# Performance work log

Hardware: AMD Instinct MI355X
Metric: run time of the kernel (lower is better)

Reference implementation:

```python
import jax, jax.numpy as jnp
import numpy as np

N_NODES = 50000
N_EDGES = 800000


def gcn_layer(x, edge_index, W, b):
    """PyG-style GCNConv: add self-loops, symmetric deg^-1/2 normalization,
    linear transform, scatter-sum aggregation at target nodes, plus bias."""
    n = x.shape[0]
    loops = jnp.arange(n)
    src = jnp.concatenate([edge_index[0], loops])  # [E+N]
    dst = jnp.concatenate([edge_index[1], loops])  # [E+N]
    deg = jax.ops.segment_sum(jnp.ones(src.shape, dtype=x.dtype), dst, num_segments=n)
    dinv = jnp.where(deg > 0, jax.lax.rsqrt(deg), jnp.zeros((), x.dtype))
    norm = dinv[src] * dinv[dst]               # [E+N]
    h = x @ W                                   # [N, out]
    msg = norm[:, None] * h[src]                # [E+N, out] gather
    out = jax.ops.segment_sum(msg, dst, num_segments=n)  # scatter-add
    return out + b


def setup_inputs() -> dict:
    key = jax.random.key(0)
    ks = jax.random.split(key, 8)
    features = jax.random.normal(ks[0], (N_NODES, 64), dtype=jnp.float32)
    edge_index1 = jax.random.randint(ks[1], (2, N_EDGES), 0, N_NODES)
    edge_index3 = jax.random.randint(ks[2], (2, N_EDGES), 0, N_NODES)
    edge_index9 = jax.random.randint(ks[3], (2, N_EDGES), 0, N_NODES)

    def glorot(k, fi, fo):
        lim = float(np.sqrt(6.0 / (fi + fo)))
        return jax.random.uniform(k, (fi, fo), minval=-lim, maxval=lim, dtype=jnp.float32)

    W1 = glorot(ks[4], 64, 64)
    W2 = glorot(ks[5], 64, 32)
    W3 = glorot(ks[6], 32, 16)
    b1 = jnp.zeros((64,), jnp.float32)
    b2 = jnp.zeros((32,), jnp.float32)
    b3 = jnp.zeros((16,), jnp.float32)
    return dict(features=features, edge_index1=edge_index1, edge_index3=edge_index3,
                edge_index9=edge_index9, W1=W1, b1=b1, W2=W2, b2=b2, W3=W3, b3=b3)


def reference(features, edge_index1, edge_index3, edge_index9, W1, b1, W2, b2, W3, b3):
    x = jax.nn.relu(gcn_layer(features, edge_index1, W1, b1))  # hop 1
    x = jax.nn.relu(gcn_layer(x, edge_index3, W2, b2))         # hop 3
    x = jax.nn.relu(gcn_layer(x, edge_index9, W3, b3))         # hop 9
    return x
```

## Files before the change

kernel.cpp:

```cpp
#include <hip/hip_runtime.h>
#include <hip/hip_fp16.h>


#define NB   256
#define NL   3
#define TB   (NB * NL)
#define CAPE 6400
#define CAPE_E (CAPE + 8)
#define CH   8192
#define P1T  512
#define EPT  (CH / P1T)
#define P2T  512

__device__ __forceinline__ void decode_chunk(int g, int nc1, int nc2,
                                             const int* s1, const int* d1, int E1,
                                             const int* s2, const int* d2, int E2,
                                             const int* s3, const int* d3, int E3,
                                             const int** src, const int** dst, int* E, int* l,
                                             int* gout) {
    if (g < nc1)            { *src = s1; *dst = d1; *E = E1; *l = 0; }
    else if (g < nc1 + nc2) { *src = s2; *dst = d2; *E = E2; *l = 1; g -= nc1; }
    else                    { *src = s3; *dst = d3; *E = E3; *l = 2; g -= nc1 + nc2; }
    *gout = g;
}

__device__ __forceinline__ void fma4(float4& a, float s, const float4& w) {
    a.x += s * w.x; a.y += s * w.y; a.z += s * w.z; a.w += s * w.w;
}
__device__ __forceinline__ void add4(float4& a, const float4& v) {
    a.x += v.x; a.y += v.y; a.z += v.z; a.w += v.w;
}
__device__ __forceinline__ float4 ldh4(const __half* h, size_t idx4) {
    uint2 r = ((const uint2*)h)[idx4];
    __half2 a = *reinterpret_cast<__half2*>(&r.x);
    __half2 b = *reinterpret_cast<__half2*>(&r.y);
    float2 fa = __half22float2(a), fb = __half22float2(b);
    return make_float4(fa.x, fa.y, fb.x, fb.y);
}
__device__ __forceinline__ void sth4(__half* h, size_t idx4, float4 v) {
    __half2 a = __floats2half2_rn(v.x, v.y);
    __half2 b = __floats2half2_rn(v.z, v.w);
    uint2 r;
    r.x = *reinterpret_cast<unsigned*>(&a);
    r.y = *reinterpret_cast<unsigned*>(&b);
    ((uint2*)h)[idx4] = r;
}

__global__ void __launch_bounds__(P1T) k1_phase1_gemm1(
        const int* __restrict__ s1, const int* __restrict__ d1, int E1,
        const int* __restrict__ s2, const int* __restrict__ d2, int E2,
        const int* __restrict__ s3, const int* __restrict__ d3, int E3,
        int nc1, int nc2, int W, int nchunks,
        int* __restrict__ gcur, unsigned int* __restrict__ pairBuf,
        const float* __restrict__ x0, const float* __restrict__ W1g,
        __half* __restrict__ h1) {
    __shared__ __align__(16) char smem[45056];
    const int t = threadIdx.x;
    if (blockIdx.x < (unsigned)nchunks) {
        int* hist = (int*)smem;
        int* eofs = hist + NB;
        int* bo   = eofs + NB;
        int* lcur = bo + NB;
        unsigned* stage = (unsigned*)(smem + 4096);
        unsigned char* stageQ = (unsigned char*)(smem + 36864);
        for (int i = t; i < NB; i += P1T) hist[i] = 0;
        __syncthreads();
        const int* src; const int* dst; int E, l, g;
        decode_chunk(blockIdx.x, nc1, nc2, s1, d1, E1, s2, d2, E2, s3, d3, E3,
                     &src, &dst, &E, &l, &g);
        const int e0 = g * CH;
        const int lbase = l * NB;
        unsigned pv[EPT];
        int bn[EPT];
        if (E - e0 >= CH) {
            const int4* s4 = (const int4*)(src + e0);
            const int4* d4 = (const int4*)(dst + e0);
#pragma unroll
            for (int w = 0; w < EPT / 4; ++w) {
                int4 sv = s4[t + w * P1T];
                int4 dv = d4[t + w * P1T];
                int q, i = w * 4;
                q = dv.x / W; bn[i+0] = q; pv[i+0] = ((unsigned)sv.x << 9) | (unsigned)(dv.x - q * W);
                q = dv.y / W; bn[i+1] = q; pv[i+1] = ((unsigned)sv.y << 9) | (unsigned)(dv.y - q * W);
                q = dv.z / W; bn[i+2] = q; pv[i+2] = ((unsigned)sv.z << 9) | (unsigned)(dv.z - q * W);
                q = dv.w / W; bn[i+3] = q; pv[i+3] = ((unsigned)sv.w << 9) | (unsigned)(dv.w - q * W);
            }
        } else {
#pragma unroll
            for (int i = 0; i < EPT; ++i) {
                int e = e0 + t + i * P1T;
                if (e < E) {
                    int s = src[e], d = dst[e];
                    int q = d / W;
                    bn[i] = q;
                    pv[i] = ((unsigned)s << 9) | (unsigned)(d - q * W);
                } else bn[i] = -1;
            }
        }
#pragma unroll
        for (int i = 0; i < EPT; ++i)
            if (bn[i] >= 0) atomicAdd(&hist[bn[i]], 1);
        __syncthreads();
        if (t < NB) eofs[t] = hist[t];
        __syncthreads();
        for (int off = 1; off < NB; off <<= 1) {
            int add = (t < NB && t >= off) ? eofs[t - off] : 0;
            __syncthreads();
            if (t < NB) eofs[t] += add;
            __syncthreads();
        }
        const int total = eofs[NB - 1];
        int excl = 0;
        if (t < NB) excl = eofs[t] - hist[t];
        __syncthreads();
        if (t < NB) {
            eofs[t] = excl;
            lcur[t] = excl;
            int c = hist[t];
            bo[t] = (lbase + t) * CAPE + (c ? atomicAdd(&gcur[lbase + t], c) : 0);
        }
        __syncthreads();
#pragma unroll
        for (int i = 0; i < EPT; ++i) {
            if (bn[i] >= 0) {
                int r = atomicAdd(&lcur[bn[i]], 1);
                stage[r] = pv[i];
                stageQ[r] = (unsigned char)bn[i];
            }
        }
        __syncthreads();
        for (int i = t; i < total; i += P1T) {
            int q = stageQ[i];
            int k = bo[q] + (i - eofs[q]);
            if (k < (lbase + q + 1) * CAPE) pairBuf[k] = stage[i];
        }
    } else {
        float* Ws = (float*)smem;
        const int bid = blockIdx.x - nchunks;
        for (int i = t; i < 1024; i += P1T)
            ((float4*)Ws)[i] = ((const float4*)W1g)[i];
        __syncthreads();
        const int tc = t % 16;
        const int tr = t / 16;
        const int row0 = bid * 128 + tr * 4;
        const float4* x4 = (const float4*)x0;
        const float4* Ws4 = (const float4*)Ws;
        float4 acc[4];
#pragma unroll
        for (int r = 0; r < 4; ++r) acc[r] = make_float4(0.f, 0.f, 0.f, 0.f);
        int rowc[4];
#pragma unroll
        for (int r = 0; r < 4; ++r) rowc[r] = min(row0 + r, 49999);
        for (int k0 = 0; k0 < 64; k0 += 4) {
            float4 wv0 = Ws4[(k0 + 0) * 16 + tc];
            float4 wv1 = Ws4[(k0 + 1) * 16 + tc];
            float4 wv2 = Ws4[(k0 + 2) * 16 + tc];
            float4 wv3 = Ws4[(k0 + 3) * 16 + tc];
#pragma unroll
            for (int r = 0; r < 4; ++r) {
                float4 xv = x4[(size_t)rowc[r] * 16 + (k0 / 4)];
                fma4(acc[r], xv.x, wv0);
                fma4(acc[r], xv.y, wv1);
                fma4(acc[r], xv.z, wv2);
                fma4(acc[r], xv.w, wv3);
            }
        }
#pragma unroll
        for (int r = 0; r < 4; ++r) {
            int row = row0 + r;
            if (row < 50000) sth4(h1, (size_t)row * 16 + tc, acc[r]);
        }
    }
}

__global__ void __launch_bounds__(P2T) k2_phase2(
        const unsigned int* __restrict__ pairBuf, const int* __restrict__ gcur,
        int n, int W,
        int* __restrict__ row_ptr, int* __restrict__ cnt_g,
        float* __restrict__ dinv, unsigned short* __restrict__ eidx,
        __half* __restrict__ h1, int* __restrict__ perm) {
    __shared__ __align__(16) char smem[20480];
    int* lcnt  = (int*)smem;
    int* lscan = lcnt + P2T;
    unsigned short* stage = (unsigned short*)(lscan + P2T);
    float* dloc = (float*)(smem + 17408);
    unsigned* sortk = (unsigned*)(smem + 19456);
    const int bid = blockIdx.x;
    const int l = bid / NB, k = bid % NB;
    const int lo = k * W;
    const int hi = min(n, lo + W);
    const int Wn = hi - lo;
    const int segE = min(gcur[bid], CAPE);
    const size_t base  = (size_t)bid * CAPE;
    const int    baseE = bid * CAPE_E;
    const int t = threadIdx.x;
    lcnt[t] = 0;
    __syncthreads();
    for (int i = t; i < segE; i += P2T)
        atomicAdd(&lcnt[pairBuf[base + i] & 511u], 1);
    __syncthreads();
    const int v = lcnt[t];
    const int vp = (v + 3) & ~3;
    lscan[t] = vp;
    __syncthreads();
    for (int off = 1; off < P2T; off <<= 1) {
        int add = (t >= off) ? lscan[t - off] : 0;
        __syncthreads();
        lscan[t] += add;
        __syncthreads();
    }
    const int pexcl = lscan[t] - vp;
    const int segEp = lscan[P2T - 1];
    if (t < Wn) {
        int node = l * n + lo + t;
        row_ptr[node] = baseE + pexcl;
        cnt_g[node] = v;
        float dv = rsqrtf((float)v + 1.0f);
        dinv[node] = dv;
        dloc[t] = dv;
    }
    __syncthreads();
    lcnt[t] = pexcl;
    __syncthreads();
    const bool lds_ok = (segEp <= CAPE);
    for (int i = t; i < segE; i += P2T) {
        unsigned p = pairBuf[base + i];
        int pos = atomicAdd(&lcnt[p & 511u], 1);
        unsigned short s = (unsigned short)(p >> 9);
        if (lds_ok) stage[pos] = s;
        else if (pos < CAPE_E) eidx[baseE + pos] = s;
    }
    __syncthreads();
    if (lds_ok) {
        const int4* st4 = (const int4*)stage;
        int4* e4 = (int4*)(eidx + baseE);
        int m16 = (segEp + 7) >> 3;
        for (int i = t; i < m16; i += P2T) e4[i] = st4[i];
    }
    if (l == 0) {
        for (int i = t; i < Wn * 16; i += P2T) {
            int r = i >> 4, c = i & 15;
            size_t idx = (size_t)(lo + r) * 16 + c;
            float4 vv = ldh4(h1, idx);
            float s = dloc[r];
            vv.x *= s; vv.y *= s; vv.z *= s; vv.w *= s;
            sth4(h1, idx, vv);
        }
    }
    if (t < 256)
        sortk[t] = (t < Wn) ? (((unsigned)min(v, 8191) << 9) | (unsigned)t)
                            : 0xFFFFFFFFu;
    for (int kk = 2; kk <= 256; kk <<= 1) {
        for (int j = kk >> 1; j > 0; j >>= 1) {
            __syncthreads();
            if (t < 256) {
                int ixj = t ^ j;
                if (ixj > t) {
                    unsigned a = sortk[t], b = sortk[ixj];
                    bool up = ((t & kk) == 0);
                    if ((a > b) == up) { sortk[t] = b; sortk[ixj] = a; }
                }
            }
        }
    }
    __syncthreads();
    if (t < Wn) perm[l * n + lo + t] = lo + (int)(sortk[t] & 511u);
}

__global__ void __launch_bounds__(256) k3_gather1_gemm2(
        const int* __restrict__ row_ptr, const int* __restrict__ cnt,
        const unsigned short* __restrict__ eidx, const float* __restrict__ dinv1,
        const float* __restrict__ dinv2, const int* __restrict__ perm,
        const __half* __restrict__ h1, const float* __restrict__ b1,
        const float* __restrict__ W2g, __half* __restrict__ h2, int n) {
    __shared__ float xs[16 * 68];
    __shared__ float W2s[64 * 32];
    for (int i = threadIdx.x; i < 512; i += 256)
        ((float4*)W2s)[i] = ((const float4*)W2g)[i];
    const int ln = threadIdx.x >> 4;
    const int f4 = threadIdx.x & 15;
    const int gidx = blockIdx.x * 16 + ln;
    const int node = (gidx < n) ? perm[gidx] : 0;
    if (gidx < n) {
        const int beg = row_ptr[node];
        const int m = cnt[node];
        float4 a0 = make_float4(0.f, 0.f, 0.f, 0.f), a1 = a0, a2 = a0, a3 = a0;
        int j = 0;
        for (; j + 8 <= m; j += 8) {
            ushort4 e0 = *(const ushort4*)(eidx + beg + j);
            ushort4 e1 = *(const ushort4*)(eidx + beg + j + 4);
            add4(a0, ldh4(h1, (size_t)e0.x * 16 + f4));
            add4(a1, ldh4(h1, (size_t)e0.y * 16 + f4));
            add4(a2, ldh4(h1, (size_t)e0.z * 16 + f4));
            add4(a3, ldh4(h1, (size_t)e0.w * 16 + f4));
            add4(a0, ldh4(h1, (size_t)e1.x * 16 + f4));
            add4(a1, ldh4(h1, (size_t)e1.y * 16 + f4));
            add4(a2, ldh4(h1, (size_t)e1.z * 16 + f4));
            add4(a3, ldh4(h1, (size_t)e1.w * 16 + f4));
        }
        if (j + 4 <= m) {
            ushort4 e0 = *(const ushort4*)(eidx + beg + j);
            add4(a0, ldh4(h1, (size_t)e0.x * 16 + f4));
            add4(a1, ldh4(h1, (size_t)e0.y * 16 + f4));
            add4(a2, ldh4(h1, (size_t)e0.z * 16 + f4));
            add4(a3, ldh4(h1, (size_t)e0.w * 16 + f4));
            j += 4;
        }
        for (; j < m; ++j)
            add4(a0, ldh4(h1, (size_t)eidx[beg + j] * 16 + f4));
        add4(a0, a1); add4(a2, a3); add4(a0, a2);
        float di = dinv1[node];
        float4 self = ldh4(h1, (size_t)node * 16 + f4);
        float4 bv = ((const float4*)b1)[f4];
        float4 o;
        o.x = di * (a0.x + self.x) + bv.x;
        o.y = di * (a0.y + self.y) + bv.y;
        o.z = di * (a0.z + self.z) + bv.z;
        o.w = di * (a0.w + self.w) + bv.w;
        o.x = o.x > 0.f ? o.x : 0.f;
        o.y = o.y > 0.f ? o.y : 0.f;
        o.z = o.z > 0.f ? o.z : 0.f;
        o.w = o.w > 0.f ? o.w : 0.f;
        *(float4*)&xs[ln * 68 + f4 * 4] = o;
    }
    __syncthreads();
    if (gidx < n) {
        const int c0 = f4 * 2;
        float s0 = 0.f, s1 = 0.f;
#pragma unroll
        for (int k = 0; k < 64; ++k) {
            float xv = xs[ln * 68 + k];
            s0 += xv * W2s[k * 32 + c0];
            s1 += xv * W2s[k * 32 + c0 + 1];
        }
        float d2 = dinv2[node];
        ((__half2*)h2)[(size_t)node * 16 + f4] = __floats2half2_rn(s0 * d2, s1 * d2);
    }
}

__global__ void __launch_bounds__(256) k4_gather2_gemm3(
        const int* __restrict__ row_ptr2, const int* __restrict__ cnt2,
        const unsigned short* __restrict__ eidx, const float* __restrict__ dinv2,
        const float* __restrict__ dinv3, const int* __restrict__ perm,
        const __half* __restrict__ h2, const float* __restrict__ b2,
        const float* __restrict__ W3g, __half* __restrict__ h3, int n) {
    __shared__ float xs[32 * 36];
    __shared__ float W3s[32 * 16];
    for (int i = threadIdx.x; i < 128; i += 256)
        ((float4*)W3s)[i] = ((const float4*)W3g)[i];
    const int ln = threadIdx.x >> 3;
    const int f4 = threadIdx.x & 7;
    const int gidx = blockIdx.x * 32 + ln;
    const int node = (gidx < n) ? perm[gidx] : 0;
    if (gidx < n) {
        const int beg = row_ptr2[node];
        const int m = cnt2[node];
        float4 a0 = make_float4(0.f, 0.f, 0.f, 0.f), a1 = a0, a2 = a0, a3 = a0;
        int j = 0;
        for (; j + 8 <= m; j += 8) {
            ushort4 e0 = *(const ushort4*)(eidx + beg + j);
            ushort4 e1 = *(const ushort4*)(eidx + beg + j + 4);
            add4(a0, ldh4(h2, (size_t)e0.x * 8 + f4));
            add4(a1, ldh4(h2, (size_t)e0.y * 8 + f4));
            add4(a2, ldh4(h2, (size_t)e0.z * 8 + f4));
            add4(a3, ldh4(h2, (size_t)e0.w * 8 + f4));
            add4(a0, ldh4(h2, (size_t)e1.x * 8 + f4));
            add4(a1, ldh4(h2, (size_t)e1.y * 8 + f4));
            add4(a2, ldh4(h2, (size_t)e1.z * 8 + f4));
            add4(a3, ldh4(h2, (size_t)e1.w * 8 + f4));
        }
        if (j + 4 <= m) {
            ushort4 e0 = *(const ushort4*)(eidx + beg + j);
            add4(a0, ldh4(h2, (size_t)e0.x * 8 + f4));
            add4(a1, ldh4(h2, (size_t)e0.y * 8 + f4));
            add4(a2, ldh4(h2, (size_t)e0.z * 8 + f4));
            add4(a3, ldh4(h2, (size_t)e0.w * 8 + f4));
            j += 4;
        }
        for (; j < m; ++j)
            add4(a0, ldh4(h2, (size_t)eidx[beg + j] * 8 + f4));
        add4(a0, a1); add4(a2, a3); add4(a0, a2);
        float di = dinv2[node];
        float4 self = ldh4(h2, (size_t)node * 8 + f4);
        float4 bv = ((const float4*)b2)[f4];
        float4 o;
        o.x = di * (a0.x + self.x) + bv.x;
        o.y = di * (a0.y + self.y) + bv.y;
        o.z = di * (a0.z + self.z) + bv.z;
        o.w = di * (a0.w + self.w) + bv.w;
        o.x = o.x > 0.f ? o.x : 0.f;
        o.y = o.y > 0.f ? o.y : 0.f;
        o.z = o.z > 0.f ? o.z : 0.f;
        o.w = o.w > 0.f ? o.w : 0.f;
        *(float4*)&xs[ln * 36 + f4 * 4] = o;
    }
    __syncthreads();
    if (gidx < n) {
        const int c0 = f4 * 2;
        float s0 = 0.f, s1 = 0.f;
#pragma unroll
        for (int k = 0; k < 32; ++k) {
            float xv = xs[ln * 36 + k];
            s0 += xv * W3s[k * 16 + c0];
            s1 += xv * W3s[k * 16 + c0 + 1];
        }
        float d3 = dinv3[node];
        ((__half2*)h3)[(size_t)node * 8 + f4] = __floats2half2_rn(s0 * d3, s1 * d3);
    }
}

__global__ void __launch_bounds__(256) k5_gather3(
        const int* __restrict__ row_ptr3, const int* __restrict__ cnt3,
        const unsigned short* __restrict__ eidx, const float* __restrict__ dinv3,
        const int* __restrict__ perm,
        const __half* __restrict__ h3, const float* __restrict__ b3,
        float* __restrict__ out, int n) {
    const int ln = threadIdx.x >> 2;
    const int f4 = threadIdx.x & 3;
    const int gidx = blockIdx.x * 64 + ln;
    if (gidx >= n) return;
    const int node = perm[gidx];
    const int beg = row_ptr3[node];
    const int m = cnt3[node];
    float4 a0 = make_float4(0.f, 0.f, 0.f, 0.f), a1 = a0, a2 = a0, a3 = a0;
    int j = 0;
    for (; j + 8 <= m; j += 8) {
        ushort4 e0 = *(const ushort4*)(eidx + beg + j);
        ushort4 e1 = *(const ushort4*)(eidx + beg + j + 4);
        add4(a0, ldh4(h3, (size_t)e0.x * 4 + f4));
        add4(a1, ldh4(h3, (size_t)e0.y * 4 + f4));
        add4(a2, ldh4(h3, (size_t)e0.z * 4 + f4));
        add4(a3, ldh4(h3, (size_t)e0.w * 4 + f4));
        add4(a0, ldh4(h3, (size_t)e1.x * 4 + f4));
        add4(a1, ldh4(h3, (size_t)e1.y * 4 + f4));
        add4(a2, ldh4(h3, (size_t)e1.z * 4 + f4));
        add4(a3, ldh4(h3, (size_t)e1.w * 4 + f4));
    }
    if (j + 4 <= m) {
        ushort4 e0 = *(const ushort4*)(eidx + beg + j);
        add4(a0, ldh4(h3, (size_t)e0.x * 4 + f4));
        add4(a1, ldh4(h3, (size_t)e0.y * 4 + f4));
        add4(a2, ldh4(h3, (size_t)e0.z * 4 + f4));
        add4(a3, ldh4(h3, (size_t)e0.w * 4 + f4));
        j += 4;
    }
    for (; j < m; ++j)
        add4(a0, ldh4(h3, (size_t)eidx[beg + j] * 4 + f4));
    add4(a0, a1); add4(a2, a3); add4(a0, a2);
    float di = dinv3[node];
    float4 self = ldh4(h3, (size_t)node * 4 + f4);
    float4 bv = ((const float4*)b3)[f4];
    float4 o;
    o.x = di * (a0.x + self.x) + bv.x;
    o.y = di * (a0.y + self.y) + bv.y;
    o.z = di * (a0.z + self.z) + bv.z;
    o.w = di * (a0.w + self.w) + bv.w;
    o.x = o.x > 0.f ? o.x : 0.f;
    o.y = o.y > 0.f ? o.y : 0.f;
    o.z = o.z > 0.f ? o.z : 0.f;
    o.w = o.w > 0.f ? o.w : 0.f;
    ((float4*)out)[(size_t)node * 4 + f4] = o;
}

extern "C" void kernel_launch(void* const* d_in, const int* in_sizes, int n_in,
                              void* d_out, int out_size, void* d_ws, size_t ws_size,
                              hipStream_t stream) {
    const float* x0  = (const float*)d_in[0];
    const int*   ei1 = (const int*)d_in[1];
    const int*   ei3 = (const int*)d_in[2];
    const int*   ei9 = (const int*)d_in[3];
    const float* W1  = (const float*)d_in[4];
    const float* b1  = (const float*)d_in[5];
    const float* W2  = (const float*)d_in[6];
    const float* b2  = (const float*)d_in[7];
    const float* W3  = (const float*)d_in[8];
    const float* b3  = (const float*)d_in[9];

    const int n  = in_sizes[0] / 64;
    const int E1 = in_sizes[1] / 2;
    const int E3 = in_sizes[2] / 2;
    const int E9 = in_sizes[3] / 2;
    const int n3 = 3 * n;
    const int W  = (n + NB - 1) / NB;

    const int nc1 = (E1 + CH - 1) / CH;
    const int nc2 = (E3 + CH - 1) / CH;
    const int nc3 = (E9 + CH - 1) / CH;
    const int nchunks = nc1 + nc2 + nc3;
    const int gemmBlks = (n + 127) / 128;

    int* gcur    = (int*)d_ws;
    unsigned int* pairBuf = (unsigned int*)(gcur + TB);
    unsigned short* eidx = (unsigned short*)(pairBuf + (size_t)TB * CAPE);
    int* row_ptr = (int*)(eidx + (size_t)TB * CAPE_E);
    int* cnt     = row_ptr + n3;
    float* dinv  = (float*)(cnt + n3);
    int* perm    = (int*)(dinv + n3);
    __half* h1   = (__half*)(perm + n3);
    __half* h2   = h1 + (size_t)n * 64;
    __half* h3   = h2 + (size_t)n * 32;

    hipMemsetAsync(gcur, 0, TB * sizeof(int), stream);
    k1_phase1_gemm1<<<nchunks + gemmBlks, P1T, 0, stream>>>(
        ei1, ei1 + E1, E1, ei3, ei3 + E3, E3, ei9, ei9 + E9, E9,
        nc1, nc2, W, nchunks, gcur, pairBuf, x0, W1, h1);
    k2_phase2<<<TB, P2T, 0, stream>>>(
        pairBuf, gcur, n, W, row_ptr, cnt, dinv, eidx, h1, perm);
    k3_gather1_gemm2<<<(n + 15) / 16, 256, 0, stream>>>(
        row_ptr, cnt, eidx, dinv, dinv + n, perm, h1, b1, W2, h2, n);
    k4_gather2_gemm3<<<(n + 31) / 32, 256, 0, stream>>>(
        row_ptr + n, cnt + n, eidx, dinv + n, dinv + 2 * n, perm + n, h2, b2, W3, h3, n);
    k5_gather3<<<(n + 63) / 64, 256, 0, stream>>>(
        row_ptr + 2 * n, cnt + 2 * n, eidx, dinv + 2 * n, perm + 2 * n, h3, b3, (float*)d_out, n);
}
```

Baseline: 160.3 us.

## Use wave-shuffle scans, counting-sort permutation, and smaller phase-1 blocks

Replaces the shared-memory Hillis-Steele prefix scans in phase 1 and phase 2 with wavefront shuffle scans plus a small per-wave sum combine, which removes many __syncthreads barriers. The bitonic sort that orders nodes by degree in phase 2 becomes a counting sort using LDS atomics and a scan. Phase 1 chunks and blocks are halved (4096 edges, 256 threads) and the GEMM1 blocks handle 64 rows, so LDS use drops and more blocks run. Within each degree bucket, ties now end up in atomic order rather than a deterministic order, and degree keys are capped at 511.

```diff
diff --git a/kernel.cpp b/kernel.cpp
--- a/kernel.cpp
+++ b/kernel.cpp
@@ -7,8 +7,8 @@
 #define TB   (NB * NL)
 #define CAPE 6400
 #define CAPE_E (CAPE + 8)
-#define CH   8192
-#define P1T  512
+#define CH   4096
+#define P1T  256
 #define EPT  (CH / P1T)
 #define P2T  512
 
@@ -46,6 +46,16 @@
     ((uint2*)h)[idx4] = r;
 }
 
+__device__ __forceinline__ int wave_incl_scan(int v) {
+    int incl = v;
+#pragma unroll
+    for (int off = 1; off < 64; off <<= 1) {
+        int u = __shfl_up(incl, (unsigned)off, 64);
+        if ((threadIdx.x & 63) >= off) incl += u;
+    }
+    return incl;
+}
+
 __global__ void __launch_bounds__(P1T) k1_phase1_gemm1(
         const int* __restrict__ s1, const int* __restrict__ d1, int E1,
         const int* __restrict__ s2, const int* __restrict__ d2, int E2,
@@ -54,7 +64,8 @@
         int* __restrict__ gcur, unsigned int* __restrict__ pairBuf,
         const float* __restrict__ x0, const float* __restrict__ W1g,
         __half* __restrict__ h1) {
-    __shared__ __align__(16) char smem[45056];
+    __shared__ __align__(16) char smem[24576];
+    __shared__ int wsum[4];
     const int t = threadIdx.x;
     if (blockIdx.x < (unsigned)nchunks) {
         int* hist = (int*)smem;
@@ -62,8 +73,8 @@
         int* bo   = eofs + NB;
         int* lcur = bo + NB;
         unsigned* stage = (unsigned*)(smem + 4096);
-        unsigned char* stageQ = (unsigned char*)(smem + 36864);
-        for (int i = t; i < NB; i += P1T) hist[i] = 0;
+        unsigned char* stageQ = (unsigned char*)(smem + 20480);
+        hist[t] = 0;
         __syncthreads();
         const int* src; const int* dst; int E, l, g;
         decode_chunk(blockIdx.x, nc1, nc2, s1, d1, E1, s2, d2, E2, s3, d3, E3,
@@ -101,24 +112,22 @@
         for (int i = 0; i < EPT; ++i)
             if (bn[i] >= 0) atomicAdd(&hist[bn[i]], 1);
         __syncthreads();
-        if (t < NB) eofs[t] = hist[t];
+        const int c = hist[t];
+        int incl = wave_incl_scan(c);
+        const int lane = t & 63, wid = t >> 6;
+        if (lane == 63) wsum[wid] = incl;
         __syncthreads();
-        for (int off = 1; off < NB; off <<= 1) {
-            int add = (t < NB && t >= off) ? eofs[t - off] : 0;
-            __syncthreads();
-            if (t < NB) eofs[t] += add;
-            __syncthreads();
-        }
-        const int total = eofs[NB - 1];
-        int excl = 0;
-        if (t < NB) excl = eofs[t] - hist[t];
-        __syncthreads();
-        if (t < NB) {
-            eofs[t] = excl;
-            lcur[t] = excl;
-            int c = hist[t];
-            bo[t] = (lbase + t) * CAPE + (c ? atomicAdd(&gcur[lbase + t], c) : 0);
-        }
+        int base = 0, total = 0;
+#pragma unroll
+        for (int w = 0; w < 4; ++w) {
+            int s = wsum[w];
+            total += s;
+            if (w < wid) base += s;
+        }
+        const int excl = base + incl - c;
+        eofs[t] = excl;
+        lcur[t] = excl;
+        bo[t] = (lbase + t) * CAPE + (c ? atomicAdd(&gcur[lbase + t], c) : 0);
         __syncthreads();
 #pragma unroll
         for (int i = 0; i < EPT; ++i) {
@@ -142,7 +151,7 @@
         __syncthreads();
         const int tc = t % 16;
         const int tr = t / 16;
-        const int row0 = bid * 128 + tr * 4;
+        const int row0 = bid * 64 + tr * 4;
         const float4* x4 = (const float4*)x0;
         const float4* Ws4 = (const float4*)Ws;
         float4 acc[4];
@@ -179,12 +188,12 @@
         int* __restrict__ row_ptr, int* __restrict__ cnt_g,
         float* __restrict__ dinv, unsigned short* __restrict__ eidx,
         __half* __restrict__ h1, int* __restrict__ perm) {
-    __shared__ __align__(16) char smem[20480];
+    __shared__ __align__(16) char smem[19456];
+    __shared__ int wsum[8];
     int* lcnt  = (int*)smem;
     int* lscan = lcnt + P2T;
     unsigned short* stage = (unsigned short*)(lscan + P2T);
     float* dloc = (float*)(smem + 17408);
-    unsigned* sortk = (unsigned*)(smem + 19456);
     const int bid = blockIdx.x;
     const int l = bid / NB, k = bid % NB;
     const int lo = k * W;
@@ -194,6 +203,7 @@
     const size_t base  = (size_t)bid * CAPE;
     const int    baseE = bid * CAPE_E;
     const int t = threadIdx.x;
+    const int lane = t & 63, wid = t >> 6;
     lcnt[t] = 0;
     __syncthreads();
     for (int i = t; i < segE; i += P2T)
@@ -201,16 +211,17 @@
     __syncthreads();
     const int v = lcnt[t];
     const int vp = (v + 3) & ~3;
-    lscan[t] = vp;
-    __syncthreads();
-    for (int off = 1; off < P2T; off <<= 1) {
-        int add = (t >= off) ? lscan[t - off] : 0;
-        __syncthreads();
-        lscan[t] += add;
-        __syncthreads();
-    }
-    const int pexcl = lscan[t] - vp;
-    const int segEp = lscan[P2T - 1];
+    int incl = wave_incl_scan(vp);
+    if (lane == 63) wsum[wid] = incl;
+    __syncthreads();
+    int sbase = 0, segEp = 0;
+#pragma unroll
+    for (int w = 0; w < 8; ++w) {
+        int s = wsum[w];
+        segEp += s;
+        if (w < wid) sbase += s;
+    }
+    const int pexcl = sbase + incl - vp;
     if (t < Wn) {
         int node = l * n + lo + t;
         row_ptr[node] = baseE + pexcl;
@@ -239,32 +250,36 @@
     }
     if (l == 0) {
         for (int i = t; i < Wn * 16; i += P2T) {
-            int r = i >> 4, c = i & 15;
-            size_t idx = (size_t)(lo + r) * 16 + c;
+            int r = i >> 4, cc = i & 15;
+            size_t idx = (size_t)(lo + r) * 16 + cc;
             float4 vv = ldh4(h1, idx);
             float s = dloc[r];
             vv.x *= s; vv.y *= s; vv.z *= s; vv.w *= s;
             sth4(h1, idx, vv);
         }
     }
-    if (t < 256)
-        sortk[t] = (t < Wn) ? (((unsigned)min(v, 8191) << 9) | (unsigned)t)
-                            : 0xFFFFFFFFu;
-    for (int kk = 2; kk <= 256; kk <<= 1) {
-        for (int j = kk >> 1; j > 0; j >>= 1) {
-            __syncthreads();
-            if (t < 256) {
-                int ixj = t ^ j;
-                if (ixj > t) {
-                    unsigned a = sortk[t], b = sortk[ixj];
-                    bool up = ((t & kk) == 0);
-                    if ((a > b) == up) { sortk[t] = b; sortk[ixj] = a; }
-                }
-            }
-        }
-    }
-    __syncthreads();
-    if (t < Wn) perm[l * n + lo + t] = lo + (int)(sortk[t] & 511u);
+    __syncthreads();
+    lcnt[t] = 0;
+    __syncthreads();
+    int key = 0, myr = 0;
+    if (t < Wn) {
+        key = min(v, 511);
+        myr = atomicAdd(&lcnt[key], 1);
+    }
+    __syncthreads();
+    const int c2 = lcnt[t];
+    int incl2 = wave_incl_scan(c2);
+    if (lane == 63) wsum[wid] = incl2;
+    __syncthreads();
+    int base2 = 0;
+#pragma unroll
+    for (int w = 0; w < 8; ++w) {
+        int s = wsum[w];
+        if (w < wid) base2 += s;
+    }
+    lscan[t] = base2 + incl2 - c2;
+    __syncthreads();
+    if (t < Wn) perm[l * n + lo + lscan[key] + myr] = lo + t;
 }
 
 __global__ void __launch_bounds__(256) k3_gather1_gemm2(
@@ -487,7 +502,7 @@
     const int nc2 = (E3 + CH - 1) / CH;
     const int nc3 = (E9 + CH - 1) / CH;
     const int nchunks = nc1 + nc2 + nc3;
-    const int gemmBlks = (n + 127) / 128;
+    const int gemmBlks = (n + 63) / 64;
 
     int* gcur    = (int*)d_ws;
     unsigned int* pairBuf = (unsigned int*)(gcur + TB);
```

Result: no change. 158.6 us, median of 2 (-1.1%).
